# Kernel optimization log

Measured on AMD Instinct MI355X. Metric: run time of the kernel, lower is better.

Reference implementation:

```python
import jax, jax.numpy as jnp
import numpy as np

EMB = 1024

def setup_inputs() -> dict:
    key = jax.random.key(0)
    ks = jax.random.split(key, 7)
    s = 1.0 / np.sqrt(EMB)
    x = jax.random.normal(ks[0], (4, 2048, EMB), dtype=jnp.float32)
    Wk = jax.random.normal(ks[1], (EMB, EMB), dtype=jnp.float32) * s
    bk = jnp.zeros((EMB,), dtype=jnp.float32)
    Wq = jax.random.normal(ks[2], (EMB, EMB), dtype=jnp.float32) * s
    bq = jnp.zeros((EMB,), dtype=jnp.float32)
    Wv = jax.random.normal(ks[3], (EMB, EMB), dtype=jnp.float32) * s
    bv = jnp.zeros((EMB,), dtype=jnp.float32)
    return {"x": x, "Wk": Wk, "bk": bk, "Wq": Wq, "bq": bq, "Wv": Wv, "bv": bv}

def reference(x, Wk, bk, Wq, bq, Wv, bv):
    # Linear layers: x @ W.T + b (torch nn.Linear convention)
    k = jnp.einsum('bse,fe->bsf', x, Wk) + bk
    q = jnp.einsum('bse,fe->bsf', x, Wq) + bq
    v = jnp.einsum('bse,fe->bsf', x, Wv) + bv
    E = x.shape[-1]
    # NOTE: original computes k @ q^T (not q @ k^T) — reproduce faithfully.
    sim = jnp.einsum('bsd,btd->bst', k, q) / jnp.sqrt(jnp.float32(E))
    S = x.shape[1]
    causal = jnp.tril(jnp.ones((S, S), dtype=bool))  # [S,S]
    sim = jnp.where(causal, sim, -jnp.inf)
    attn = jax.nn.softmax(sim, axis=-1)
    return jnp.einsum('bst,btd->bsd', attn, v)
```

## Files before the change

### kernel.cpp

```cpp
#include <hip/hip_runtime.h>
#include <cstdint>


typedef __attribute__((ext_vector_type(8))) _Float16 f16x8;
typedef __attribute__((ext_vector_type(4))) float f32x4;

__device__ __forceinline__ unsigned short f2h(float x) {
  return __builtin_bit_cast(unsigned short, (_Float16)x);
}

__device__ __forceinline__ void lds_dma16(const void* g, void* l) {
  auto gp = reinterpret_cast<const __attribute__((address_space(1))) void*>(
      reinterpret_cast<uintptr_t>(g));
  auto lp = reinterpret_cast<__attribute__((address_space(3))) void*>(
      reinterpret_cast<uintptr_t>(l));
  __builtin_amdgcn_global_load_lds(gp, lp, 16, 0, 0);
}

__device__ __forceinline__ void stage_half(const unsigned short* __restrict__ G,
                                           int ld, unsigned short* lds,
                                           int tid) {
  const int r = tid >> 3;
  const int c = ((tid & 7) ^ (r & 7)) * 8;
  lds_dma16(G + (size_t)r * ld + c, lds + tid * 8);
  lds_dma16(G + (size_t)(r + 64) * ld + c, lds + 4096 + tid * 8);
}

__device__ __forceinline__ void gemm256(
    const unsigned short* __restrict__ Ag, const unsigned short* __restrict__ Bg,
    int lda, int ldb, int nk, unsigned short* As, unsigned short* Bs,
    f32x4 (&acc)[8][4]) {
  const int tid = threadIdx.x;
  const int lane = tid & 63, wave = tid >> 6;
  const int wr = wave >> 2, wc = wave & 3;
  const int rr = lane & 15, qq = lane >> 4;
  const int s7 = rr & 7;
  const int soff0 = (qq ^ s7) * 8;
  const int soff1 = ((4 + qq) ^ s7) * 8;
  const int aoff = wr * 8192 + rr * 64;
  const int boff = (wc >> 1) * 8192 + (wc & 1) * 4096 + rr * 64;

#pragma unroll
  for (int fi = 0; fi < 8; ++fi)
#pragma unroll
    for (int fj = 0; fj < 4; ++fj) {
      f32x4 z = {0.f, 0.f, 0.f, 0.f};
      acc[fi][fj] = z;
    }

  stage_half(Ag, lda, As, tid);
  stage_half(Ag + (size_t)128 * lda, lda, As + 8192, tid);
  stage_half(Bg, ldb, Bs, tid);
  stage_half(Bg + (size_t)128 * ldb, ldb, Bs + 8192, tid);
  asm volatile("s_waitcnt vmcnt(0)" ::: "memory");
  __builtin_amdgcn_s_barrier();

  for (int k0 = 0; k0 < nk; k0 += 128) {
    const bool last = (k0 + 128 >= nk);
#pragma unroll
    for (int P = 0; P < 4; ++P) {
      const int b = P >> 1;
      if (P == 0) {
        stage_half(Ag + (k0 + 64), lda, As + 16384, tid);
        stage_half(Ag + (size_t)128 * lda + (k0 + 64), lda, As + 24576, tid);
      } else if (P == 1) {
        stage_half(Bg + (k0 + 64), ldb, Bs + 16384, tid);
        stage_half(Bg + (size_t)128 * ldb + (k0 + 64), ldb, Bs + 24576, tid);
      } else if (!last) {
        if (P == 2) {
          stage_half(Ag + (k0 + 128), lda, As, tid);
          stage_half(Ag + (size_t)128 * lda + (k0 + 128), lda, As + 8192, tid);
        } else {
          stage_half(Bg + (k0 + 128), ldb, Bs, tid);
          stage_half(Bg + (size_t)128 * ldb + (k0 + 128), ldb, Bs + 8192, tid);
        }
      }
      const int so = (P & 1) ? soff1 : soff0;
      const unsigned short* Ar = As + b * 16384 + aoff + so;
      const unsigned short* Br = Bs + b * 16384 + boff + so;
      f16x8 af[8], bf[4];
#pragma unroll
      for (int fi = 0; fi < 8; ++fi) af[fi] = *(const f16x8*)(Ar + fi * 1024);
#pragma unroll
      for (int fj = 0; fj < 4; ++fj) bf[fj] = *(const f16x8*)(Br + fj * 1024);
      asm volatile("s_waitcnt lgkmcnt(8)" ::: "memory");
      __builtin_amdgcn_s_barrier();
      asm volatile("s_waitcnt lgkmcnt(0)" ::: "memory");
      __builtin_amdgcn_sched_barrier(0);
      __builtin_amdgcn_s_setprio(1);
#pragma unroll
      for (int fi = 0; fi < 8; ++fi)
#pragma unroll
        for (int fj = 0; fj < 4; ++fj)
          acc[fi][fj] = __builtin_amdgcn_mfma_f32_16x16x32_f16(
              af[fi], bf[fj], acc[fi][fj], 0, 0, 0);
      __builtin_amdgcn_s_setprio(0);
      if (P == 1) {
        asm volatile("s_waitcnt vmcnt(0)" ::: "memory");
      } else if (P == 3 && !last) {
        asm volatile("s_waitcnt vmcnt(0)" ::: "memory");
      }
      __builtin_amdgcn_s_barrier();
    }
  }
}

__device__ __forceinline__ void gemm128_k64(
    const unsigned short* __restrict__ Ag, const unsigned short* __restrict__ Bg,
    int lda, int ldb, int nk, unsigned short* As, unsigned short* Bs,
    f32x4 acc[4][4]) {
  const int tid = threadIdx.x;
  const int lane = tid & 63, wave = tid >> 6;
  const int wm = wave >> 1, wn = wave & 1;
  const int sr = lane >> 3;
  const int scb = ((lane & 7) ^ sr) * 8;
  const int rr = lane & 15, qq = lane >> 4;
  const int slot0 = ((qq) ^ (rr & 7)) * 8;
  const int slot1 = ((4 + qq) ^ (rr & 7)) * 8;

#pragma unroll
  for (int i = 0; i < 4; ++i)
#pragma unroll
    for (int j = 0; j < 4; ++j) {
      f32x4 z = {0.f, 0.f, 0.f, 0.f};
      acc[i][j] = z;
    }

#pragma unroll
  for (int c = 0; c < 4; ++c) {
    int chunk = wave * 4 + c;
    int row = chunk * 8 + sr;
    lds_dma16(Ag + (size_t)row * lda + scb, As + chunk * 512);
    lds_dma16(Bg + (size_t)row * ldb + scb, Bs + chunk * 512);
  }

  int buf = 0;
  for (int k0 = 0; k0 < nk; k0 += 64) {
    __syncthreads();
    const int kn = k0 + 64;
    if (kn < nk) {
      unsigned short* An = As + (buf ^ 1) * 8192;
      unsigned short* Bn = Bs + (buf ^ 1) * 8192;
#pragma unroll
      for (int c = 0; c < 4; ++c) {
        int chunk = wave * 4 + c;
        int row = chunk * 8 + sr;
        lds_dma16(Ag + (size_t)row * lda + kn + scb, An + chunk * 512);
        lds_dma16(Bg + (size_t)row * ldb + kn + scb, Bn + chunk * 512);
      }
    }

    const unsigned short* Ar = As + buf * 8192 + (wm * 64 + rr) * 64;
    const unsigned short* Br = Bs + buf * 8192 + (wn * 64 + rr) * 64;
    {
      f16x8 af[4], bf[4];
#pragma unroll
      for (int i = 0; i < 4; ++i) af[i] = *(const f16x8*)(Ar + i * 1024 + slot0);
#pragma unroll
      for (int j = 0; j < 4; ++j) bf[j] = *(const f16x8*)(Br + j * 1024 + slot0);
#pragma unroll
      for (int i = 0; i < 4; ++i)
#pragma unroll
        for (int j = 0; j < 4; ++j)
          acc[i][j] = __builtin_amdgcn_mfma_f32_16x16x32_f16(af[i], bf[j],
                                                             acc[i][j], 0, 0, 0);
    }
    {
      f16x8 af[4], bf[4];
#pragma unroll
      for (int i = 0; i < 4; ++i) af[i] = *(const f16x8*)(Ar + i * 1024 + slot1);
#pragma unroll
      for (int j = 0; j < 4; ++j) bf[j] = *(const f16x8*)(Br + j * 1024 + slot1);
#pragma unroll
      for (int i = 0; i < 4; ++i)
#pragma unroll
        for (int j = 0; j < 4; ++j)
          acc[i][j] = __builtin_amdgcn_mfma_f32_16x16x32_f16(af[i], bf[j],
                                                             acc[i][j], 0, 0, 0);
    }
    buf ^= 1;
  }
}

__global__ void cvt_kernel(const float* __restrict__ x,
                           const float* __restrict__ w0,
                           const float* __restrict__ w1,
                           const float* __restrict__ w2,
                           unsigned short* __restrict__ dst,
                           float* __restrict__ rsum) {
  int i = blockIdx.x * 256 + threadIdx.x;
  if (i >= 2883584) {
    int z2 = i - 2883584;
    float4 z = {0.f, 0.f, 0.f, 0.f};
    ((float4*)rsum)[z2] = z;
    return;
  }
  const float* s;
  size_t si;
  if (i < 2097152) {
    s = x; si = i;
  } else {
    int j = i - 2097152;
    int z = j >> 18;
    s = (z == 0) ? w0 : ((z == 1) ? w1 : w2);
    si = j & 262143;
  }
  float4 f = ((const float4*)s)[si];
  ushort4 u;
  u.x = f2h(f.x); u.y = f2h(f.y); u.z = f2h(f.z); u.w = f2h(f.w);
  ((ushort4*)dst)[i] = u;
}

__global__ __launch_bounds__(512, 2) void qkv256_kernel(
    const unsigned short* __restrict__ xh, const unsigned short* __restrict__ wh,
    const float* __restrict__ bk, const float* __restrict__ bq,
    const float* __restrict__ bv, unsigned short* __restrict__ kh,
    unsigned short* __restrict__ qh, unsigned short* __restrict__ vT) {
  __shared__ unsigned short As[32768], Bs[32768];
  const int job = (blockIdx.x & 7) * 48 + (blockIdx.x >> 3);

  const unsigned short* Ag;
  const unsigned short* Bg;
  if (job < 256) {
    const int tm = job >> 3, tn = job & 7;
    Ag = xh + (size_t)tm * 256 * 1024;
    Bg = wh + (size_t)tn * 256 * 1024;
  } else {
    const int j = job - 256;
    const int dt = j >> 5, tt = j & 31;
    Ag = wh + 2097152 + (size_t)dt * 256 * 1024;
    Bg = xh + (size_t)tt * 256 * 1024;
  }

  f32x4 acc[8][4];
  gemm256(Ag, Bg, 1024, 1024, 1024, As, Bs, acc);

  const int tid = threadIdx.x;
  const int lane = tid & 63, wave = tid >> 6;
  const int wr = wave >> 2, wc = wave & 3, rr = lane & 15, qq = lane >> 4;

  if (job < 256) {
    const int tm = job >> 3, tn = job & 7;
    const bool isq = tn >= 4;
    unsigned short* dst = isq ? qh : kh;
    const float* bias = isq ? bq : bk;
    const int nbase = (tn & 3) * 256;
    float bj[4];
#pragma unroll
    for (int fj = 0; fj < 4; ++fj)
      bj[fj] = bias[nbase + wc * 64 + fj * 16 + rr];
#pragma unroll
    for (int fi = 0; fi < 8; ++fi)
#pragma unroll
      for (int reg = 0; reg < 4; ++reg) {
        const int m = tm * 256 + wr * 128 + fi * 16 + qq * 4 + reg;
#pragma unroll
        for (int fj = 0; fj < 4; ++fj) {
          const int n = nbase + wc * 64 + fj * 16 + rr;
          dst[(size_t)m * 1024 + n] = f2h(acc[fi][fj][reg] + bj[fj]);
        }
      }
  } else {
    const int j = job - 256;
    const int dt = j >> 5, tt = j & 31;
#pragma unroll
    for (int fi = 0; fi < 8; ++fi) {
      const int d0 = dt * 256 + wr * 128 + fi * 16 + qq * 4;
      const float4 b4 = *(const float4*)(bv + d0);
      const float bir[4] = {b4.x, b4.y, b4.z, b4.w};
#pragma unroll
      for (int reg = 0; reg < 4; ++reg) {
        const int d = d0 + reg;
#pragma unroll
        for (int fj = 0; fj < 4; ++fj) {
          const int tg = tt * 256 + wc * 64 + fj * 16 + rr;
          const int bb = tg >> 11, t = tg & 2047;
          vT[((size_t)(bb * 1024 + d)) * 2048 + t] =
              f2h(acc[fi][fj][reg] + bir[reg]);
        }
      }
    }
  }
}

__global__ __launch_bounds__(256) void scores_kernel(
    const unsigned short* __restrict__ kh, const unsigned short* __restrict__ qh,
    unsigned short* __restrict__ P, float* __restrict__ rsum) {
  const int b = blockIdx.y;
  int idx = blockIdx.x;
  int ts = (int)((sqrtf(8.0f * idx + 1.0f) - 1.0f) * 0.5f);
  while ((ts + 1) * (ts + 2) / 2 <= idx) ++ts;
  while (ts * (ts + 1) / 2 > idx) --ts;
  const int tt = idx - ts * (ts + 1) / 2;
  __shared__ unsigned short As[2 * 128 * 64], Bs[2 * 128 * 64];

  f32x4 acc[4][4];
  gemm128_k64(kh + ((size_t)(b * 2048 + ts * 128)) * 1024,
              qh + ((size_t)(b * 2048 + tt * 128)) * 1024,
              1024, 1024, 1024, As, Bs, acc);

  const int lane = threadIdx.x & 63, wave = threadIdx.x >> 6;
  const int wm = wave >> 1, wn = wave & 1, rr = lane & 15, qq = lane >> 4;
  unsigned short* Pb = P + (size_t)b * 2048 * 2048;
  float* rs = rsum + b * 2048;
#pragma unroll
  for (int i = 0; i < 4; ++i)
#pragma unroll
    for (int reg = 0; reg < 4; ++reg) {
      int srow = ts * 128 + wm * 64 + i * 16 + qq * 4 + reg;
      float p = 0.f;
#pragma unroll
      for (int j = 0; j < 4; ++j) {
        int tcol = tt * 128 + wn * 64 + j * 16 + rr;
        float e = (tcol <= srow) ? __expf(acc[i][j][reg] * 0.03125f - 4.0f)
                                 : 0.0f;
        Pb[(size_t)srow * 2048 + tcol] = f2h(e);
        p += e;
      }
#pragma unroll
      for (int off = 1; off < 16; off <<= 1) p += __shfl_xor(p, off);
      if (rr == 0) atomicAdd(rs + srow, p);
    }
}

__global__ __launch_bounds__(256) void pv_gemm_kernel(
    const unsigned short* __restrict__ P, const unsigned short* __restrict__ vT,
    const float* __restrict__ rsum, float* __restrict__ out) {
  const int td = blockIdx.x, ts = 15 - blockIdx.y, b = blockIdx.z;
  __shared__ unsigned short As[2 * 128 * 64], Bs[2 * 128 * 64];

  f32x4 acc[4][4];
  gemm128_k64(P + ((size_t)(b * 2048 + ts * 128)) * 2048,
              vT + ((size_t)(b * 1024 + td * 128)) * 2048,
              2048, 2048, (ts + 1) * 128, As, Bs, acc);

  const int lane = threadIdx.x & 63, wave = threadIdx.x >> 6;
  const int wm = wave >> 1, wn = wave & 1, rr = lane & 15, qq = lane >> 4;
#pragma unroll
  for (int i = 0; i < 4; ++i) {
    int s0 = ts * 128 + wm * 64 + i * 16 + qq * 4;
    float4 r4 = *(const float4*)(rsum + b * 2048 + s0);
    float rv[4] = {__builtin_amdgcn_rcpf(r4.x), __builtin_amdgcn_rcpf(r4.y),
                   __builtin_amdgcn_rcpf(r4.z), __builtin_amdgcn_rcpf(r4.w)};
#pragma unroll
    for (int reg = 0; reg < 4; ++reg) {
      int srow = s0 + reg;
#pragma unroll
      for (int j = 0; j < 4; ++j) {
        int dcol = td * 128 + wn * 64 + j * 16 + rr;
        out[((size_t)(b * 2048 + srow)) * 1024 + dcol] =
            acc[i][j][reg] * rv[reg];
      }
    }
  }
}

extern "C" void kernel_launch(void* const* d_in, const int* in_sizes, int n_in,
                              void* d_out, int out_size, void* d_ws,
                              size_t ws_size, hipStream_t stream) {
  const float* x  = (const float*)d_in[0];
  const float* Wk = (const float*)d_in[1];
  const float* bk = (const float*)d_in[2];
  const float* Wq = (const float*)d_in[3];
  const float* bq = (const float*)d_in[4];
  const float* Wv = (const float*)d_in[5];
  const float* bv = (const float*)d_in[6];
  float* out = (float*)d_out;

  char* ws = (char*)d_ws;
  const size_t MB = 1ull << 20;
  unsigned short* xh = (unsigned short*)(ws + 0);
  unsigned short* wh = (unsigned short*)(ws + 16 * MB);
  unsigned short* P  = (unsigned short*)(ws + 0);
  unsigned short* kh = (unsigned short*)(ws + 38 * MB);
  unsigned short* qh = (unsigned short*)(ws + 54 * MB);
  unsigned short* vT = (unsigned short*)(ws + 70 * MB);
  float* rsum = (float*)(ws + 86 * MB);

  cvt_kernel<<<11272, 256, 0, stream>>>(x, Wk, Wq, Wv, xh, rsum);
  qkv256_kernel<<<384, 512, 0, stream>>>(xh, wh, bk, bq, bv, kh, qh, vT);
  scores_kernel<<<dim3(136, 4), 256, 0, stream>>>(kh, qh, P, rsum);
  pv_gemm_kernel<<<dim3(8, 16, 4), 256, 0, stream>>>(P, vT, rsum, out);
}
```

Measured before the change: 244.5 us.

## Restructure 256x256 GEMM staging into 4-stage ring of 32-wide K slices

Replaces the double-buffered 64-wide K staging (loaded in halves) with a four-slot ring buffer of 32-wide K slices, prefetching three slices ahead. The LDS swizzle changes from an 8-way to a 4-way XOR to match the 32-element rows. The goal is deeper global-to-LDS prefetch and finer-grained overlap of DMA with MFMA. In exchange each barrier now covers half as much MFMA work, so there are more barriers per K, and the 4-way swizzle may cause more LDS bank conflicts.

```diff
diff --git a/kernel.cpp b/kernel.cpp
--- a/kernel.cpp
+++ b/kernel.cpp
@@ -17,13 +17,15 @@
   __builtin_amdgcn_global_load_lds(gp, lp, 16, 0, 0);
 }
 
-__device__ __forceinline__ void stage_half(const unsigned short* __restrict__ G,
-                                           int ld, unsigned short* lds,
-                                           int tid) {
-  const int r = tid >> 3;
-  const int c = ((tid & 7) ^ (r & 7)) * 8;
-  lds_dma16(G + (size_t)r * ld + c, lds + tid * 8);
-  lds_dma16(G + (size_t)(r + 64) * ld + c, lds + 4096 + tid * 8);
+__device__ __forceinline__ void stage32(const unsigned short* __restrict__ G,
+                                        int ld, unsigned short* lds, int tid) {
+#pragma unroll
+  for (int d = 0; d < 2; ++d) {
+    const int u = d * 512 + tid;
+    const int r = u >> 2, s = u & 3;
+    const int c = (s ^ (r & 3)) * 8;
+    lds_dma16(G + (size_t)r * ld + c, lds + u * 8);
+  }
 }
 
 __device__ __forceinline__ void gemm256(
@@ -34,11 +36,9 @@
   const int lane = tid & 63, wave = tid >> 6;
   const int wr = wave >> 2, wc = wave & 3;
   const int rr = lane & 15, qq = lane >> 4;
-  const int s7 = rr & 7;
-  const int soff0 = (qq ^ s7) * 8;
-  const int soff1 = ((4 + qq) ^ s7) * 8;
-  const int aoff = wr * 8192 + rr * 64;
-  const int boff = (wc >> 1) * 8192 + (wc & 1) * 4096 + rr * 64;
+  const int soff = (qq ^ (rr & 3)) * 8;
+  const int aoff = (wr * 128 + rr) * 32 + soff;
+  const int boff = (wc * 64 + rr) * 32 + soff;
 
 #pragma unroll
   for (int fi = 0; fi < 8; ++fi)
@@ -48,60 +48,48 @@
       acc[fi][fj] = z;
     }
 
-  stage_half(Ag, lda, As, tid);
-  stage_half(Ag + (size_t)128 * lda, lda, As + 8192, tid);
-  stage_half(Bg, ldb, Bs, tid);
-  stage_half(Bg + (size_t)128 * ldb, ldb, Bs + 8192, tid);
-  asm volatile("s_waitcnt vmcnt(0)" ::: "memory");
+  const int NS = nk >> 5;
+  stage32(Ag, lda, As, tid);
+  stage32(Bg, ldb, Bs, tid);
+  stage32(Ag + 32, lda, As + 8192, tid);
+  stage32(Bg + 32, ldb, Bs + 8192, tid);
+  stage32(Ag + 64, lda, As + 16384, tid);
+  stage32(Bg + 64, ldb, Bs + 16384, tid);
+  asm volatile("s_waitcnt vmcnt(8)" ::: "memory");
   __builtin_amdgcn_s_barrier();
 
-  for (int k0 = 0; k0 < nk; k0 += 128) {
-    const bool last = (k0 + 128 >= nk);
-#pragma unroll
-    for (int P = 0; P < 4; ++P) {
-      const int b = P >> 1;
-      if (P == 0) {
-        stage_half(Ag + (k0 + 64), lda, As + 16384, tid);
-        stage_half(Ag + (size_t)128 * lda + (k0 + 64), lda, As + 24576, tid);
-      } else if (P == 1) {
-        stage_half(Bg + (k0 + 64), ldb, Bs + 16384, tid);
-        stage_half(Bg + (size_t)128 * ldb + (k0 + 64), ldb, Bs + 24576, tid);
-      } else if (!last) {
-        if (P == 2) {
-          stage_half(Ag + (k0 + 128), lda, As, tid);
-          stage_half(Ag + (size_t)128 * lda + (k0 + 128), lda, As + 8192, tid);
-        } else {
-          stage_half(Bg + (k0 + 128), ldb, Bs, tid);
-          stage_half(Bg + (size_t)128 * ldb + (k0 + 128), ldb, Bs + 8192, tid);
-        }
-      }
-      const int so = (P & 1) ? soff1 : soff0;
-      const unsigned short* Ar = As + b * 16384 + aoff + so;
-      const unsigned short* Br = Bs + b * 16384 + boff + so;
-      f16x8 af[8], bf[4];
-#pragma unroll
-      for (int fi = 0; fi < 8; ++fi) af[fi] = *(const f16x8*)(Ar + fi * 1024);
-#pragma unroll
-      for (int fj = 0; fj < 4; ++fj) bf[fj] = *(const f16x8*)(Br + fj * 1024);
-      asm volatile("s_waitcnt lgkmcnt(8)" ::: "memory");
-      __builtin_amdgcn_s_barrier();
-      asm volatile("s_waitcnt lgkmcnt(0)" ::: "memory");
-      __builtin_amdgcn_sched_barrier(0);
-      __builtin_amdgcn_s_setprio(1);
-#pragma unroll
-      for (int fi = 0; fi < 8; ++fi)
-#pragma unroll
-        for (int fj = 0; fj < 4; ++fj)
-          acc[fi][fj] = __builtin_amdgcn_mfma_f32_16x16x32_f16(
-              af[fi], bf[fj], acc[fi][fj], 0, 0, 0);
-      __builtin_amdgcn_s_setprio(0);
-      if (P == 1) {
-        asm volatile("s_waitcnt vmcnt(0)" ::: "memory");
-      } else if (P == 3 && !last) {
-        asm volatile("s_waitcnt vmcnt(0)" ::: "memory");
-      }
-      __builtin_amdgcn_s_barrier();
-    }
+  for (int s = 0; s < NS; ++s) {
+    if (s + 3 < NS) {
+      stage32(Ag + (size_t)(s + 3) * 32, lda, As + ((s + 3) & 3) * 8192, tid);
+      stage32(Bg + (size_t)(s + 3) * 32, ldb, Bs + ((s + 3) & 3) * 8192, tid);
+    }
+    const unsigned short* Ar = As + (s & 3) * 8192 + aoff;
+    const unsigned short* Br = Bs + (s & 3) * 8192 + boff;
+    f16x8 af[8], bf[4];
+#pragma unroll
+    for (int fi = 0; fi < 8; ++fi) af[fi] = *(const f16x8*)(Ar + fi * 512);
+#pragma unroll
+    for (int fj = 0; fj < 4; ++fj) bf[fj] = *(const f16x8*)(Br + fj * 512);
+    asm volatile("s_waitcnt lgkmcnt(8)" ::: "memory");
+    __builtin_amdgcn_s_barrier();
+    asm volatile("s_waitcnt lgkmcnt(0)" ::: "memory");
+    __builtin_amdgcn_sched_barrier(0);
+    __builtin_amdgcn_s_setprio(1);
+#pragma unroll
+    for (int fi = 0; fi < 8; ++fi)
+#pragma unroll
+      for (int fj = 0; fj < 4; ++fj)
+        acc[fi][fj] = __builtin_amdgcn_mfma_f32_16x16x32_f16(
+            af[fi], bf[fj], acc[fi][fj], 0, 0, 0);
+    __builtin_amdgcn_s_setprio(0);
+    if (s < NS - 3) {
+      asm volatile("s_waitcnt vmcnt(8)" ::: "memory");
+    } else if (s == NS - 3) {
+      asm volatile("s_waitcnt vmcnt(4)" ::: "memory");
+    } else if (s == NS - 2) {
+      asm volatile("s_waitcnt vmcnt(0)" ::: "memory");
+    }
+    __builtin_amdgcn_s_barrier();
   }
 }
 
```

Result: no change. 249.4 us (+2.0%).
